# Kernel optimization log

Hardware: AMD Instinct MI355X
Metric: run time of the kernel (lower is better)

The kernel has to match this reference:

```python
import jax, jax.numpy as jnp
import numpy as np

N_NODES = 50000
N_EDGES = 800000
F_IN = 128
HID = 64
HEADS = 4
CLASSES = 40
NEG_SLOPE = 0.2
EPS = 1e-16


def glorot(key, shape):
    fan_in, fan_out = shape[0], shape[-1]
    lim = jnp.sqrt(6.0 / (fan_in + fan_out))
    return jax.random.uniform(key, shape, jnp.float32, -lim, lim)


def setup_inputs() -> dict:
    key = jax.random.key(0)
    ks = jax.random.split(key, 10)
    x = jax.random.normal(ks[0], (N_NODES, F_IN), jnp.float32)
    edge_index = jax.random.randint(ks[1], (2, N_EDGES), 0, N_NODES, jnp.int64)
    # layer 1: F_IN -> HID per head, HEADS heads, concat
    W1 = glorot(ks[2], (F_IN, HEADS * HID))
    a_src1 = glorot(ks[3], (1, HEADS, HID))
    a_dst1 = glorot(ks[4], (1, HEADS, HID))
    b1 = jnp.zeros((HEADS * HID,), jnp.float32)
    # layer 2: HEADS*HID -> CLASSES, 1 head
    W2 = glorot(ks[5], (HEADS * HID, CLASSES))
    a_src2 = glorot(ks[6], (1, 1, CLASSES))
    a_dst2 = glorot(ks[7], (1, 1, CLASSES))
    b2 = jnp.zeros((CLASSES,), jnp.float32)
    return {"x": x, "edge_index": edge_index, "W1": W1, "a_src1": a_src1,
            "a_dst1": a_dst1, "b1": b1, "W2": W2, "a_src2": a_src2,
            "a_dst2": a_dst2, "b2": b2}


def gat_conv(x, src, dst, W, a_src, a_dst, bias, heads, out_dim):
    n = x.shape[0]
    h = (x @ W).reshape(n, heads, out_dim)           # [N,H,D]
    alpha_s = jnp.sum(h * a_src, axis=-1)            # [N,H]
    alpha_d = jnp.sum(h * a_dst, axis=-1)            # [N,H]
    e = alpha_s[src] + alpha_d[dst]                  # [E,H]
    e = jax.nn.leaky_relu(e, NEG_SLOPE)
    # segment softmax over edges grouped by destination node
    m = jax.ops.segment_max(e, dst, num_segments=n)  # [N,H]
    ex = jnp.exp(e - m[dst])
    denom = jax.ops.segment_sum(ex, dst, num_segments=n)
    alpha = ex / (denom[dst] + EPS)                  # [E,H]
    msg = h[src] * alpha[:, :, None]                 # [E,H,D]
    out = jax.ops.segment_sum(msg, dst, num_segments=n)
    return out.reshape(n, heads * out_dim) + bias


def reference(x, edge_index, W1, a_src1, a_dst1, b1, W2, a_src2, a_dst2, b2):
    src, dst = edge_index[0], edge_index[1]
    h = gat_conv(x, src, dst, W1, a_src1, a_dst1, b1, HEADS, HID)
    h = jax.nn.relu(h)
    h = gat_conv(h, src, dst, W2, a_src2, a_dst2, b2, 1, CLASSES)
    return jax.nn.log_softmax(h, axis=1)
```

## Files before the change

### kernel.cpp

```cpp
#include <hip/hip_runtime.h>
#include <math.h>

#define NN 50000
#define NE 800000
#define FIN 128
#define HID 64
#define HEADS 4
#define C1 256
#define CLS 40
#define EPSF 1e-16f

#define NB 98
#define BSH 9
#define BSTRIDE 9216
#define NBLK_B 625
#define CHUNK 1280

typedef __attribute__((ext_vector_type(8))) short bf16x8;
typedef __attribute__((ext_vector_type(4))) float f32x4;
typedef __attribute__((ext_vector_type(2))) float f32x2;

__device__ __forceinline__ unsigned short f2bf(float f) {
    unsigned int u = __float_as_uint(f);
    unsigned int r = (u + 0x7fffu + ((u >> 16) & 1u)) >> 16;
    return (unsigned short)r;
}
__device__ __forceinline__ float bflo(unsigned int u) { return __uint_as_float(u << 16); }
__device__ __forceinline__ float bfhi(unsigned int u) { return __uint_as_float(u & 0xffff0000u); }
__device__ __forceinline__ unsigned char f2fp8(float v) {
    int pk = __builtin_amdgcn_cvt_pk_fp8_f32(v, v, 0, false);
    return (unsigned char)(pk & 0xff);
}
__device__ __forceinline__ float lrelu(float e) { return e > 0.f ? e : 0.2f * e; }

__global__ __launch_bounds__(512) void k_bucket(const int* __restrict__ ei,
                                                int* __restrict__ gcur,
                                                unsigned int* __restrict__ stage,
                                                const float* __restrict__ W1,
                                                const float* __restrict__ W2,
                                                unsigned short* __restrict__ wB1,
                                                unsigned short* __restrict__ wB2) {
    __shared__ unsigned int lchunk[CHUNK];
    __shared__ unsigned int lsort[CHUNK];
    __shared__ int lhist[128];
    __shared__ int sbuf[128];
    __shared__ int lstart[128];
    __shared__ int lbase[128];
    __shared__ int lcur[128];
    int t = threadIdx.x;

    if (blockIdx.x < 11) {
        int tw = blockIdx.x * 512 + t;
        if (tw < 4096) {
            int tn = tw >> 8;
            int kc = (tw >> 6) & 3;
            int lw = tw & 63;
            int n = tn * 16 + (lw & 15);
            int k0 = kc * 32 + (lw >> 4) * 8;
            unsigned short* o = wB1 + (size_t)tw * 8;
#pragma unroll
            for (int j = 0; j < 8; j++) o[j] = f2bf(W1[(size_t)(k0 + j) * C1 + n]);
        } else if (tw < 4096 + 1536) {
            int u = tw - 4096;
            int tn = u >> 9;
            int kc = (u >> 6) & 7;
            int lw = u & 63;
            int n = tn * 16 + (lw & 15);
            int k0 = kc * 32 + (lw >> 4) * 8;
            unsigned short* o = wB2 + (size_t)u * 8;
#pragma unroll
            for (int j = 0; j < 8; j++)
                o[j] = (n < CLS) ? f2bf(W2[(size_t)(k0 + j) * CLS + n]) : (unsigned short)0;
        }
    }

    int e0 = blockIdx.x * CHUNK;
    if (t < 128) lhist[t] = 0;
    __syncthreads();
    for (int j = t; j < CHUNK; j += 512) {
        int s = ei[e0 + j];
        int d = ei[NE + e0 + j];
        int b = d >> BSH;
        atomicAdd(&lhist[b], 1);
        lchunk[j] = (unsigned int)s | ((unsigned int)(d & 511) << 16) |
                    ((unsigned int)b << 25);
    }
    __syncthreads();
    if (t < 128) sbuf[t] = lhist[t];
    __syncthreads();
    for (int d = 1; d < 128; d <<= 1) {
        int x = (t < 128 && t >= d) ? sbuf[t - d] : 0;
        __syncthreads();
        if (t < 128) sbuf[t] += x;
        __syncthreads();
    }
    if (t < 128) {
        int excl = sbuf[t] - lhist[t];
        lstart[t] = excl;
        lcur[t] = excl;
        if (t < NB) lbase[t] = atomicAdd(&gcur[t], lhist[t]);
    }
    __syncthreads();
    for (int j = t; j < CHUNK; j += 512) {
        unsigned int pk = lchunk[j];
        int b = pk >> 25;
        int pos = atomicAdd(&lcur[b], 1);
        lsort[pos] = pk;
    }
    __syncthreads();
    for (int j = t; j < CHUNK; j += 512) {
        unsigned int pk = lsort[j];
        int b = pk >> 25;
        int dest = lbase[b] + (j - lstart[b]);
        stage[(size_t)b * BSTRIDE + dest] = pk & 0x01FFFFFFu;
    }
}

__global__ __launch_bounds__(512) void k_bsort(const unsigned int* __restrict__ stage,
                                               const int* __restrict__ gcur,
                                               int* __restrict__ offs,
                                               int* __restrict__ ssrc) {
    __shared__ int lhist[512];
    __shared__ int cur[512];
    __shared__ int sbuf[128];
    int t = threadIdx.x;
    int b = blockIdx.x;
    int cnt = gcur[b];
    const unsigned int* sp = stage + (size_t)b * BSTRIDE;
    if (t < 128) sbuf[t] = (t < NB) ? gcur[t] : 0;
    lhist[t] = 0;
    __syncthreads();
    for (int d = 1; d < 128; d <<= 1) {
        int x = (t < 128 && t >= d) ? sbuf[t - d] : 0;
        __syncthreads();
        if (t < 128) sbuf[t] += x;
        __syncthreads();
    }
    int gbase = sbuf[b] - cnt;
    for (int j = t; j < cnt; j += 512) atomicAdd(&lhist[(sp[j] >> 16) & 511], 1);
    __syncthreads();
    if (t < 64) {
        int base = t * 8;
        int vals[8];
        int run = 0;
#pragma unroll
        for (int j = 0; j < 8; j++) { int v = lhist[base + j]; vals[j] = run; run += v; }
        int sc = run;
#pragma unroll
        for (int d = 1; d < 64; d <<= 1) { int u = __shfl_up(sc, d); if (t >= d) sc += u; }
        int excl = sc - run;
#pragma unroll
        for (int j = 0; j < 8; j++) cur[base + j] = excl + vals[j];
    }
    __syncthreads();
    offs[(b << BSH) + t] = gbase + cur[t];
    __syncthreads();
    for (int j = t; j < cnt; j += 512) {
        unsigned int v = sp[j];
        int dl = (v >> 16) & 511;
        int pos = atomicAdd(&cur[dl], 1);
        ssrc[gbase + pos] = (int)(v & 0xFFFFu);
    }
}

__global__ __launch_bounds__(256) void k_gemm1(const float* __restrict__ x,
                                               const unsigned short* __restrict__ wB,
                                               const float* __restrict__ aws,
                                               const float* __restrict__ awd,
                                               unsigned char* __restrict__ h1f8,
                                               float* __restrict__ as1,
                                               float* __restrict__ ad1) {
    __shared__ uint4 Af[4][4][64];
    int t = threadIdx.x;
    int m0 = blockIdx.x * 64;
    int l = t & 63;
    int wv = t >> 6;

    bf16x8 bf[4][4];
    const bf16x8* wb = (const bf16x8*)wB + l;
#pragma unroll
    for (int tn = 0; tn < 4; tn++)
#pragma unroll
        for (int kc = 0; kc < 4; kc++)
            bf[tn][kc] = wb[(((wv * 4 + tn) * 4 + kc)) * 64];

#pragma unroll
    for (int i = 0; i < 8; i++) {
        int g = i * 256 + t;
        int row = g >> 5;
        int c4 = g & 31;
        int grow = m0 + row;
        if (grow >= NN) grow = NN - 1;
        float4 v = *(const float4*)(x + (size_t)grow * FIN + c4 * 4);
        uint2 pk;
        pk.x = (unsigned int)f2bf(v.x) | ((unsigned int)f2bf(v.y) << 16);
        pk.y = (unsigned int)f2bf(v.z) | ((unsigned int)f2bf(v.w) << 16);
        int kc = c4 >> 3;
        int rem = (c4 & 7) * 4;
        int q = rem >> 3;
        int hh = (rem >> 2) & 1;
        int ll = q * 16 + (row & 15);
        int mt = row >> 4;
        ((uint2*)&Af[mt][kc][ll])[hh] = pk;
    }
    __syncthreads();

    int q = l >> 4;
    int c = l & 15;

#pragma unroll
    for (int mt = 0; mt < 4; mt++) {
        bf16x8 a[4];
#pragma unroll
        for (int kc = 0; kc < 4; kc++) a[kc] = *(const bf16x8*)&Af[mt][kc][l];

        f32x4 acc[4];
#pragma unroll
        for (int tn = 0; tn < 4; tn++) acc[tn] = (f32x4){0.f, 0.f, 0.f, 0.f};
#pragma unroll
        for (int tn = 0; tn < 4; tn++) {
            acc[tn] = __builtin_amdgcn_mfma_f32_16x16x32_bf16(a[0], bf[tn][0], acc[tn], 0, 0, 0);
            acc[tn] = __builtin_amdgcn_mfma_f32_16x16x32_bf16(a[1], bf[tn][1], acc[tn], 0, 0, 0);
            acc[tn] = __builtin_amdgcn_mfma_f32_16x16x32_bf16(a[2], bf[tn][2], acc[tn], 0, 0, 0);
            acc[tn] = __builtin_amdgcn_mfma_f32_16x16x32_bf16(a[3], bf[tn][3], acc[tn], 0, 0, 0);
        }

        int row0 = m0 + mt * 16 + q * 4;
        float ps[4] = {0.f, 0.f, 0.f, 0.f}, pd[4] = {0.f, 0.f, 0.f, 0.f};
#pragma unroll
        for (int tn = 0; tn < 4; tn++) {
            int col = wv * 64 + tn * 16 + c;
            float wsv = aws[col];
            float wdv = awd[col];
#pragma unroll
            for (int r = 0; r < 4; r++) {
                float v = acc[tn][r];
                int row = row0 + r;
                if (row < NN) h1f8[(size_t)row * C1 + col] = f2fp8(v);
                ps[r] = fmaf(v, wsv, ps[r]);
                pd[r] = fmaf(v, wdv, pd[r]);
            }
        }
#pragma unroll
        for (int r = 0; r < 4; r++) {
            float a_ = ps[r], d_ = pd[r];
#pragma unroll
            for (int s = 1; s < 16; s <<= 1) {
                a_ += __shfl_xor(a_, s);
                d_ += __shfl_xor(d_, s);
            }
            int row = row0 + r;
            if (c == 0 && row < NN) {
                as1[row * 4 + wv] = a_;
                ad1[row * 4 + wv] = d_;
            }
        }
    }
}

__global__ __launch_bounds__(256) void k_agg1(const unsigned char* __restrict__ h1f8,
                                              const float* __restrict__ as1,
                                              const float* __restrict__ ad1,
                                              const int* __restrict__ offs,
                                              const int* __restrict__ ssrc,
                                              const float* __restrict__ b1,
                                              unsigned short* __restrict__ g1b) {
    int lane = threadIdx.x & 63;
    int half = lane >> 5;
    int hl = lane & 31;
    int head = hl >> 3;
    int node = blockIdx.x * 4 + (threadIdx.x >> 6);
    int beg = offs[node];
    int end = (node + 1 < NN) ? offs[node + 1] : NE;
    float adv = ad1[node * 4 + head];
    float l = 0.f;
    float acc[8];
#pragma unroll
    for (int c = 0; c < 8; c++) acc[c] = 0.f;
    const uint2* hv = (const uint2*)h1f8;

    if (beg < end) {
        int idx[4];
#pragma unroll
        for (int i = 0; i < 4; i++) idx[i] = ssrc[beg + 2 * i + half];
        uint2 hbA[2];
        float pA[2];
#pragma unroll
        for (int i = 0; i < 2; i++) {
            hbA[i] = hv[(size_t)idx[i] * 32 + hl];
            int e = beg + 2 * i + half;
            float p = __expf(lrelu(as1[idx[i] * 4 + head] + adv));
            pA[i] = (e < end) ? p : 0.f;
        }
        for (int j = beg; j < end; j += 8) {
            int idxN[4];
#pragma unroll
            for (int i = 0; i < 4; i++) idxN[i] = ssrc[j + 8 + 2 * i + half];
            uint2 hbB[2];
            float pB[2];
#pragma unroll
            for (int i = 0; i < 2; i++) {
                hbB[i] = hv[(size_t)idx[2 + i] * 32 + hl];
                int e = j + 4 + 2 * i + half;
                float p = __expf(lrelu(as1[idx[2 + i] * 4 + head] + adv));
                pB[i] = (e < end) ? p : 0.f;
            }
#pragma unroll
            for (int i = 0; i < 2; i++) {
                float p = pA[i];
                f32x2 v0 = __builtin_amdgcn_cvt_pk_f32_fp8(hbA[i].x, false);
                f32x2 v1 = __builtin_amdgcn_cvt_pk_f32_fp8(hbA[i].x, true);
                f32x2 v2 = __builtin_amdgcn_cvt_pk_f32_fp8(hbA[i].y, false);
                f32x2 v3 = __builtin_amdgcn_cvt_pk_f32_fp8(hbA[i].y, true);
                l += p;
                acc[0] = fmaf(p, v0.x, acc[0]);
                acc[1] = fmaf(p, v0.y, acc[1]);
                acc[2] = fmaf(p, v1.x, acc[2]);
                acc[3] = fmaf(p, v1.y, acc[3]);
                acc[4] = fmaf(p, v2.x, acc[4]);
                acc[5] = fmaf(p, v2.y, acc[5]);
                acc[6] = fmaf(p, v3.x, acc[6]);
                acc[7] = fmaf(p, v3.y, acc[7]);
            }
#pragma unroll
            for (int i = 0; i < 2; i++) {
                hbA[i] = hv[(size_t)idxN[i] * 32 + hl];
                int e = j + 8 + 2 * i + half;
                float p = __expf(lrelu(as1[idxN[i] * 4 + head] + adv));
                pA[i] = (e < end) ? p : 0.f;
            }
#pragma unroll
            for (int i = 0; i < 2; i++) {
                float p = pB[i];
                f32x2 v0 = __builtin_amdgcn_cvt_pk_f32_fp8(hbB[i].x, false);
                f32x2 v1 = __builtin_amdgcn_cvt_pk_f32_fp8(hbB[i].x, true);
                f32x2 v2 = __builtin_amdgcn_cvt_pk_f32_fp8(hbB[i].y, false);
                f32x2 v3 = __builtin_amdgcn_cvt_pk_f32_fp8(hbB[i].y, true);
                l += p;
                acc[0] = fmaf(p, v0.x, acc[0]);
                acc[1] = fmaf(p, v0.y, acc[1]);
                acc[2] = fmaf(p, v1.x, acc[2]);
                acc[3] = fmaf(p, v1.y, acc[3]);
                acc[4] = fmaf(p, v2.x, acc[4]);
                acc[5] = fmaf(p, v2.y, acc[5]);
                acc[6] = fmaf(p, v3.x, acc[6]);
                acc[7] = fmaf(p, v3.y, acc[7]);
            }
#pragma unroll
            for (int i = 0; i < 4; i++) idx[i] = idxN[i];
        }
    }
    l += __shfl_xor(l, 32);
#pragma unroll
    for (int c = 0; c < 8; c++) acc[c] += __shfl_xor(acc[c], 32);

    if (half == 0) {
        float inv = 1.f / (l + EPSF);
        const float4* b1v = (const float4*)b1;
        float4 b0 = b1v[hl * 2];
        float4 b1_ = b1v[hl * 2 + 1];
        float o[8];
        o[0] = fmaxf(fmaf(acc[0], inv, b0.x), 0.f);
        o[1] = fmaxf(fmaf(acc[1], inv, b0.y), 0.f);
        o[2] = fmaxf(fmaf(acc[2], inv, b0.z), 0.f);
        o[3] = fmaxf(fmaf(acc[3], inv, b0.w), 0.f);
        o[4] = fmaxf(fmaf(acc[4], inv, b1_.x), 0.f);
        o[5] = fmaxf(fmaf(acc[5], inv, b1_.y), 0.f);
        o[6] = fmaxf(fmaf(acc[6], inv, b1_.z), 0.f);
        o[7] = fmaxf(fmaf(acc[7], inv, b1_.w), 0.f);
        uint4 ob;
        ob.x = (unsigned int)f2bf(o[0]) | ((unsigned int)f2bf(o[1]) << 16);
        ob.y = (unsigned int)f2bf(o[2]) | ((unsigned int)f2bf(o[3]) << 16);
        ob.z = (unsigned int)f2bf(o[4]) | ((unsigned int)f2bf(o[5]) << 16);
        ob.w = (unsigned int)f2bf(o[6]) | ((unsigned int)f2bf(o[7]) << 16);
        ((uint4*)g1b)[(size_t)node * 32 + hl] = ob;
    }
}

__global__ __launch_bounds__(256) void k_gemm2(const unsigned short* __restrict__ g1b,
                                               const unsigned short* __restrict__ wB2,
                                               const float* __restrict__ aws,
                                               const float* __restrict__ awd,
                                               unsigned short* __restrict__ h2b,
                                               float* __restrict__ as2,
                                               float* __restrict__ ad2) {
    __shared__ uint4 Af[4][8][64];
    int t = threadIdx.x;
    int m0 = blockIdx.x * 64;

#pragma unroll
    for (int i = 0; i < 8; i++) {
        int g = i * 256 + t;
        int row = g >> 5;
        int c8 = g & 31;
        int grow = m0 + row;
        if (grow >= NN) grow = NN - 1;
        uint4 v = *(const uint4*)(g1b + (size_t)grow * C1 + c8 * 8);
        int kc = c8 >> 2;
        int q = c8 & 3;
        Af[row >> 4][kc][q * 16 + (row & 15)] = v;
    }
    __syncthreads();

    int l = t & 63;
    int wv = t >> 6;

    bf16x8 a[8];
#pragma unroll
    for (int kc = 0; kc < 8; kc++) a[kc] = *(const bf16x8*)&Af[wv][kc][l];

    f32x4 acc[3];
#pragma unroll
    for (int tn = 0; tn < 3; tn++) acc[tn] = (f32x4){0.f, 0.f, 0.f, 0.f};

    const bf16x8* wb = (const bf16x8*)wB2 + l;
#pragma unroll
    for (int tn = 0; tn < 3; tn++) {
#pragma unroll
        for (int kc = 0; kc < 8; kc++) {
            bf16x8 b = wb[(tn * 8 + kc) * 64];
            acc[tn] = __builtin_amdgcn_mfma_f32_16x16x32_bf16(a[kc], b, acc[tn], 0, 0, 0);
        }
    }

    int q = l >> 4;
    int c = l & 15;
    int row0 = m0 + wv * 16 + q * 4;
    float ps[4] = {0.f, 0.f, 0.f, 0.f}, pd[4] = {0.f, 0.f, 0.f, 0.f};
#pragma unroll
    for (int tn = 0; tn < 3; tn++) {
        int col = tn * 16 + c;
        bool cok = col < CLS;
        float wsv = cok ? aws[col] : 0.f;
        float wdv = cok ? awd[col] : 0.f;
#pragma unroll
        for (int r = 0; r < 4; r++) {
            float v = acc[tn][r];
            int row = row0 + r;
            if (cok && row < NN) h2b[(size_t)row * CLS + col] = f2bf(v);
            ps[r] = fmaf(v, wsv, ps[r]);
            pd[r] = fmaf(v, wdv, pd[r]);
        }
    }
#pragma unroll
    for (int r = 0; r < 4; r++) {
        float a_ = ps[r], d_ = pd[r];
#pragma unroll
        for (int s = 1; s < 16; s <<= 1) {
            a_ += __shfl_xor(a_, s);
            d_ += __shfl_xor(d_, s);
        }
        int row = row0 + r;
        if (c == 0 && row < NN) {
            as2[row] = a_;
            ad2[row] = d_;
        }
    }
}

__global__ __launch_bounds__(256) void k_agg2(const unsigned short* __restrict__ h2b,
                                              const float* __restrict__ as2,
                                              const float* __restrict__ ad2,
                                              const int* __restrict__ offs,
                                              const int* __restrict__ ssrc,
                                              const float* __restrict__ b2,
                                              float* __restrict__ out) {
    int lane = threadIdx.x & 63;
    int half = lane >> 5;
    int hl = lane & 31;
    int cl = hl < 20 ? hl : 19;
    int node = blockIdx.x * 4 + (threadIdx.x >> 6);
    int beg = offs[node];
    int end = (node + 1 < NN) ? offs[node + 1] : NE;
    float adv = ad2[node];
    float l = 0.f, aL = 0.f, aH = 0.f;
    const unsigned int* hv = (const unsigned int*)h2b;

    if (beg < end) {
        int idx[4];
#pragma unroll
        for (int i = 0; i < 4; i++) idx[i] = ssrc[beg + 2 * i + half];
        unsigned int hbA[2];
        float pA[2];
#pragma unroll
        for (int i = 0; i < 2; i++) {
            hbA[i] = hv[(size_t)idx[i] * 20 + cl];
            int e = beg + 2 * i + half;
            float p = __expf(lrelu(as2[idx[i]] + adv));
            pA[i] = (e < end) ? p : 0.f;
        }
        for (int j = beg; j < end; j += 8) {
            int idxN[4];
#pragma unroll
            for (int i = 0; i < 4; i++) idxN[i] = ssrc[j + 8 + 2 * i + half];
            unsigned int hbB[2];
            float pB[2];
#pragma unroll
            for (int i = 0; i < 2; i++) {
                hbB[i] = hv[(size_t)idx[2 + i] * 20 + cl];
                int e = j + 4 + 2 * i + half;
                float p = __expf(lrelu(as2[idx[2 + i]] + adv));
                pB[i] = (e < end) ? p : 0.f;
            }
#pragma unroll
            for (int i = 0; i < 2; i++) {
                float p = pA[i];
                l += p;
                aL = fmaf(p, bflo(hbA[i]), aL);
                aH = fmaf(p, bfhi(hbA[i]), aH);
            }
#pragma unroll
            for (int i = 0; i < 2; i++) {
                hbA[i] = hv[(size_t)idxN[i] * 20 + cl];
                int e = j + 8 + 2 * i + half;
                float p = __expf(lrelu(as2[idxN[i]] + adv));
                pA[i] = (e < end) ? p : 0.f;
            }
#pragma unroll
            for (int i = 0; i < 2; i++) {
                float p = pB[i];
                l += p;
                aL = fmaf(p, bflo(hbB[i]), aL);
                aH = fmaf(p, bfhi(hbB[i]), aH);
            }
#pragma unroll
            for (int i = 0; i < 4; i++) idx[i] = idxN[i];
        }
    }
    l += __shfl_xor(l, 32);
    aL += __shfl_xor(aL, 32);
    aH += __shfl_xor(aH, 32);

    if (half == 0) {
        bool act = hl < 20;
        float inv = 1.f / (l + EPSF);
        float vL = -INFINITY, vH = -INFINITY;
        if (act) {
            float2 b = ((const float2*)b2)[cl];
            vL = aL * inv + b.x;
            vH = aH * inv + b.y;
        }
        float mx = fmaxf(vL, vH);
#pragma unroll
        for (int s = 16; s >= 1; s >>= 1) mx = fmaxf(mx, __shfl_xor(mx, s));
        float ex = act ? (__expf(vL - mx) + __expf(vH - mx)) : 0.f;
#pragma unroll
        for (int s = 16; s >= 1; s >>= 1) ex += __shfl_xor(ex, s);
        if (act) {
            float ls = __logf(ex);
            float2 o = {vL - mx - ls, vH - mx - ls};
            *(float2*)(out + (size_t)node * CLS + cl * 2) = o;
        }
    }
}


extern "C" void kernel_launch(void* const* d_in, const int* in_sizes, int n_in,
                              void* d_out, int out_size, void* d_ws, size_t ws_size,
                              hipStream_t stream) {
    const float* x    = (const float*)d_in[0];
    const int*   ei   = (const int*)d_in[1];
    const float* W1   = (const float*)d_in[2];
    const float* as1w = (const float*)d_in[3];
    const float* ad1w = (const float*)d_in[4];
    const float* b1   = (const float*)d_in[5];
    const float* W2   = (const float*)d_in[6];
    const float* as2w = (const float*)d_in[7];
    const float* ad2w = (const float*)d_in[8];
    const float* b2   = (const float*)d_in[9];
    float* out = (float*)d_out;

    char* p = (char*)d_ws;
    auto alloc = [&](size_t bytes) {
        char* r = p;
        p += (bytes + 255) & ~(size_t)255;
        return r;
    };
    unsigned char* h1f8 = (unsigned char*)alloc((size_t)NN * C1);
    unsigned short* g1b = (unsigned short*)alloc((size_t)NN * C1 * 2);
    unsigned short* h2b = (unsigned short*)alloc((size_t)NN * CLS * 2);
    float* as1  = (float*)alloc((size_t)NN * 4 * 4);
    float* ad1  = (float*)alloc((size_t)NN * 4 * 4);
    float* as2  = (float*)alloc((size_t)NN * 4);
    float* ad2  = (float*)alloc((size_t)NN * 4);
    int* offs   = (int*)alloc((size_t)(NN + 1024) * 4);
    int* gcur   = (int*)alloc(128 * 4);
    unsigned int* stage = (unsigned int*)alloc((size_t)NB * BSTRIDE * 4);
    int* ssrc   = (int*)alloc((size_t)(NE + 64) * 4);
    unsigned short* wB1 = (unsigned short*)alloc((size_t)4096 * 8 * 2);
    unsigned short* wB2 = (unsigned short*)alloc((size_t)1536 * 8 * 2);

    hipMemsetAsync(gcur, 0, 128 * 4, stream);
    hipMemsetAsync(ssrc + NE, 0, 64 * 4, stream);

    k_bucket<<<NBLK_B, 512, 0, stream>>>(ei, gcur, stage, W1, W2, wB1, wB2);
    k_bsort<<<NB, 512, 0, stream>>>(stage, gcur, offs, ssrc);

    k_gemm1<<<(NN + 63) / 64, 256, 0, stream>>>(x, wB1, as1w, ad1w, h1f8, as1, ad1);
    k_agg1<<<NN / 4, 256, 0, stream>>>(h1f8, as1, ad1, offs, ssrc, b1, g1b);

    k_gemm2<<<(NN + 63) / 64, 256, 0, stream>>>(g1b, wB2, as2w, ad2w, h2b, as2, ad2);
    k_agg2<<<NN / 4, 256, 0, stream>>>(h2b, as2, ad2, offs, ssrc, b2, out);
}
```

Before: 213.9 us.

## Split layer-1 aggregation per head and pin each head to an XCD pair

The layer-1 aggregation now launches one wave per (node, head) instead of one wave per node covering all heads. The block index is decoded so that all blocks for a given head land on the same pair of XCDs, which keeps each head's 64-byte slice of the fp8 feature table resident in those XCDs' L2. Each wave processes 8 edges per iteration with 8 lanes per edge, then reduces across lane groups with shuffles. The cost is four times as many blocks, repeated loads of offsets, edge indices and attention scores for every head, and extra shuffle reductions.

```diff
diff --git a/kernel.cpp b/kernel.cpp
--- a/kernel.cpp
+++ b/kernel.cpp
@@ -266,99 +266,67 @@
                                               const float* __restrict__ b1,
                                               unsigned short* __restrict__ g1b) {
     int lane = threadIdx.x & 63;
-    int half = lane >> 5;
-    int hl = lane & 31;
-    int head = hl >> 3;
-    int node = blockIdx.x * 4 + (threadIdx.x >> 6);
+    int g = lane >> 3;
+    int c = lane & 7;
+    int bid = blockIdx.x;
+    int xcd = bid & 7;
+    int head = xcd >> 1;
+    int quad = (bid >> 3) * 2 + (bid & 1);
+    int node = quad * 4 + (threadIdx.x >> 6);
     int beg = offs[node];
     int end = (node + 1 < NN) ? offs[node + 1] : NE;
     float adv = ad1[node * 4 + head];
     float l = 0.f;
     float acc[8];
 #pragma unroll
-    for (int c = 0; c < 8; c++) acc[c] = 0.f;
-    const uint2* hv = (const uint2*)h1f8;
+    for (int k = 0; k < 8; k++) acc[k] = 0.f;
+    const uint2* hv = (const uint2*)(h1f8 + head * 64);
+
+#define ACC1(hb, p)                                                       \
+    {                                                                     \
+        f32x2 v;                                                          \
+        v = __builtin_amdgcn_cvt_pk_f32_fp8((hb).x, false);               \
+        acc[0] = fmaf(p, v.x, acc[0]); acc[1] = fmaf(p, v.y, acc[1]);     \
+        v = __builtin_amdgcn_cvt_pk_f32_fp8((hb).x, true);                \
+        acc[2] = fmaf(p, v.x, acc[2]); acc[3] = fmaf(p, v.y, acc[3]);     \
+        v = __builtin_amdgcn_cvt_pk_f32_fp8((hb).y, false);               \
+        acc[4] = fmaf(p, v.x, acc[4]); acc[5] = fmaf(p, v.y, acc[5]);     \
+        v = __builtin_amdgcn_cvt_pk_f32_fp8((hb).y, true);                \
+        acc[6] = fmaf(p, v.x, acc[6]); acc[7] = fmaf(p, v.y, acc[7]);     \
+        l += p;                                                           \
+    }
 
     if (beg < end) {
-        int idx[4];
-#pragma unroll
-        for (int i = 0; i < 4; i++) idx[i] = ssrc[beg + 2 * i + half];
-        uint2 hbA[2];
-        float pA[2];
-#pragma unroll
-        for (int i = 0; i < 2; i++) {
-            hbA[i] = hv[(size_t)idx[i] * 32 + hl];
-            int e = beg + 2 * i + half;
-            float p = __expf(lrelu(as1[idx[i] * 4 + head] + adv));
-            pA[i] = (e < end) ? p : 0.f;
-        }
+        int eA = beg + g;
+        int iA = ssrc[eA];
+        uint2 hA = hv[(size_t)iA * 32 + c];
+        float pA = (eA < end) ? __expf(lrelu(as1[iA * 4 + head] + adv)) : 0.f;
         for (int j = beg; j < end; j += 8) {
-            int idxN[4];
-#pragma unroll
-            for (int i = 0; i < 4; i++) idxN[i] = ssrc[j + 8 + 2 * i + half];
-            uint2 hbB[2];
-            float pB[2];
-#pragma unroll
-            for (int i = 0; i < 2; i++) {
-                hbB[i] = hv[(size_t)idx[2 + i] * 32 + hl];
-                int e = j + 4 + 2 * i + half;
-                float p = __expf(lrelu(as1[idx[2 + i] * 4 + head] + adv));
-                pB[i] = (e < end) ? p : 0.f;
-            }
-#pragma unroll
-            for (int i = 0; i < 2; i++) {
-                float p = pA[i];
-                f32x2 v0 = __builtin_amdgcn_cvt_pk_f32_fp8(hbA[i].x, false);
-                f32x2 v1 = __builtin_amdgcn_cvt_pk_f32_fp8(hbA[i].x, true);
-                f32x2 v2 = __builtin_amdgcn_cvt_pk_f32_fp8(hbA[i].y, false);
-                f32x2 v3 = __builtin_amdgcn_cvt_pk_f32_fp8(hbA[i].y, true);
-                l += p;
-                acc[0] = fmaf(p, v0.x, acc[0]);
-                acc[1] = fmaf(p, v0.y, acc[1]);
-                acc[2] = fmaf(p, v1.x, acc[2]);
-                acc[3] = fmaf(p, v1.y, acc[3]);
-                acc[4] = fmaf(p, v2.x, acc[4]);
-                acc[5] = fmaf(p, v2.y, acc[5]);
-                acc[6] = fmaf(p, v3.x, acc[6]);
-                acc[7] = fmaf(p, v3.y, acc[7]);
-            }
-#pragma unroll
-            for (int i = 0; i < 2; i++) {
-                hbA[i] = hv[(size_t)idxN[i] * 32 + hl];
-                int e = j + 8 + 2 * i + half;
-                float p = __expf(lrelu(as1[idxN[i] * 4 + head] + adv));
-                pA[i] = (e < end) ? p : 0.f;
-            }
-#pragma unroll
-            for (int i = 0; i < 2; i++) {
-                float p = pB[i];
-                f32x2 v0 = __builtin_amdgcn_cvt_pk_f32_fp8(hbB[i].x, false);
-                f32x2 v1 = __builtin_amdgcn_cvt_pk_f32_fp8(hbB[i].x, true);
-                f32x2 v2 = __builtin_amdgcn_cvt_pk_f32_fp8(hbB[i].y, false);
-                f32x2 v3 = __builtin_amdgcn_cvt_pk_f32_fp8(hbB[i].y, true);
-                l += p;
-                acc[0] = fmaf(p, v0.x, acc[0]);
-                acc[1] = fmaf(p, v0.y, acc[1]);
-                acc[2] = fmaf(p, v1.x, acc[2]);
-                acc[3] = fmaf(p, v1.y, acc[3]);
-                acc[4] = fmaf(p, v2.x, acc[4]);
-                acc[5] = fmaf(p, v2.y, acc[5]);
-                acc[6] = fmaf(p, v3.x, acc[6]);
-                acc[7] = fmaf(p, v3.y, acc[7]);
-            }
-#pragma unroll
-            for (int i = 0; i < 4; i++) idx[i] = idxN[i];
-        }
-    }
+            int eB = j + 8 + g;
+            int iB = ssrc[eB];
+            uint2 hB = hv[(size_t)iB * 32 + c];
+            float pB = (eB < end) ? __expf(lrelu(as1[iB * 4 + head] + adv)) : 0.f;
+            ACC1(hA, pA);
+            hA = hB;
+            pA = pB;
+        }
+    }
+#undef ACC1
+#pragma unroll
+    for (int k = 0; k < 8; k++) acc[k] += __shfl_xor(acc[k], 8);
+    l += __shfl_xor(l, 8);
+#pragma unroll
+    for (int k = 0; k < 8; k++) acc[k] += __shfl_xor(acc[k], 16);
+    l += __shfl_xor(l, 16);
+#pragma unroll
+    for (int k = 0; k < 8; k++) acc[k] += __shfl_xor(acc[k], 32);
     l += __shfl_xor(l, 32);
-#pragma unroll
-    for (int c = 0; c < 8; c++) acc[c] += __shfl_xor(acc[c], 32);
-
-    if (half == 0) {
+
+    if (g == 0) {
         float inv = 1.f / (l + EPSF);
         const float4* b1v = (const float4*)b1;
-        float4 b0 = b1v[hl * 2];
-        float4 b1_ = b1v[hl * 2 + 1];
+        float4 b0 = b1v[head * 16 + c * 2];
+        float4 b1_ = b1v[head * 16 + c * 2 + 1];
         float o[8];
         o[0] = fmaxf(fmaf(acc[0], inv, b0.x), 0.f);
         o[1] = fmaxf(fmaf(acc[1], inv, b0.y), 0.f);
@@ -373,7 +341,7 @@
         ob.y = (unsigned int)f2bf(o[2]) | ((unsigned int)f2bf(o[3]) << 16);
         ob.z = (unsigned int)f2bf(o[4]) | ((unsigned int)f2bf(o[5]) << 16);
         ob.w = (unsigned int)f2bf(o[6]) | ((unsigned int)f2bf(o[7]) << 16);
-        ((uint4*)g1b)[(size_t)node * 32 + hl] = ob;
+        ((uint4*)g1b)[(size_t)node * 32 + head * 8 + c] = ob;
     }
 }
 
@@ -597,7 +565,7 @@
     k_bsort<<<NB, 512, 0, stream>>>(stage, gcur, offs, ssrc);
 
     k_gemm1<<<(NN + 63) / 64, 256, 0, stream>>>(x, wB1, as1w, ad1w, h1f8, as1, ad1);
-    k_agg1<<<NN / 4, 256, 0, stream>>>(h1f8, as1, ad1, offs, ssrc, b1, g1b);
+    k_agg1<<<(NN / 4) * HEADS, 256, 0, stream>>>(h1f8, as1, ad1, offs, ssrc, b1, g1b);
 
     k_gemm2<<<(NN + 63) / 64, 256, 0, stream>>>(g1b, wB2, as2w, ad2w, h2b, as2, ad2);
     k_agg2<<<NN / 4, 256, 0, stream>>>(h2b, as2, ad2, offs, ssrc, b2, out);
```

Result: slower. 282.3 us (+31.9%).

## Merge bucket sort and first GEMM into one heterogeneous launch

Applied to the files above, without the earlier changes.

Fuses the per-bucket CSR sort kernel and the layer-1 GEMM into a single launch. The first NB blocks do the sort and the rest do GEMM tiles, two 64-row tiles per 512-thread block, with a shared-memory union covering both roles. The aim is to run the small 98-block sort alongside the independent GEMM and save one launch gap. The GEMM path now uses 512-thread blocks, which may change occupancy, and its trailing block reads clamped rows past NN.

```diff
diff --git a/kernel.cpp b/kernel.cpp
--- a/kernel.cpp
+++ b/kernel.cpp
@@ -15,6 +15,7 @@
 #define BSTRIDE 9216
 #define NBLK_B 625
 #define CHUNK 1280
+#define NBLK_G 391
 
 typedef __attribute__((ext_vector_type(8))) short bf16x8;
 typedef __attribute__((ext_vector_type(4))) float f32x4;
@@ -116,63 +117,67 @@
     }
 }
 
-__global__ __launch_bounds__(512) void k_bsort(const unsigned int* __restrict__ stage,
-                                               const int* __restrict__ gcur,
-                                               int* __restrict__ offs,
-                                               int* __restrict__ ssrc) {
-    __shared__ int lhist[512];
-    __shared__ int cur[512];
-    __shared__ int sbuf[128];
-    int t = threadIdx.x;
-    int b = blockIdx.x;
-    int cnt = gcur[b];
-    const unsigned int* sp = stage + (size_t)b * BSTRIDE;
-    if (t < 128) sbuf[t] = (t < NB) ? gcur[t] : 0;
-    lhist[t] = 0;
-    __syncthreads();
-    for (int d = 1; d < 128; d <<= 1) {
-        int x = (t < 128 && t >= d) ? sbuf[t - d] : 0;
+__global__ __launch_bounds__(512) void k_bsg(const unsigned int* __restrict__ stage,
+                                             const int* __restrict__ gcur,
+                                             int* __restrict__ offs,
+                                             int* __restrict__ ssrc,
+                                             const float* __restrict__ x,
+                                             const unsigned short* __restrict__ wB,
+                                             const float* __restrict__ aws,
+                                             const float* __restrict__ awd,
+                                             unsigned char* __restrict__ h1f8,
+                                             float* __restrict__ as1,
+                                             float* __restrict__ ad1) {
+    __shared__ union SM {
+        struct { int lhist[512]; int cur[512]; int sbuf[128]; } b;
+        struct { uint4 Af[2][4][4][64]; } g;
+    } sm;
+
+    if (blockIdx.x < NB) {
+        int t = threadIdx.x;
+        int b = blockIdx.x;
+        int cnt = gcur[b];
+        const unsigned int* sp = stage + (size_t)b * BSTRIDE;
+        if (t < 128) sm.b.sbuf[t] = (t < NB) ? gcur[t] : 0;
+        sm.b.lhist[t] = 0;
         __syncthreads();
-        if (t < 128) sbuf[t] += x;
+        for (int d = 1; d < 128; d <<= 1) {
+            int xv = (t < 128 && t >= d) ? sm.b.sbuf[t - d] : 0;
+            __syncthreads();
+            if (t < 128) sm.b.sbuf[t] += xv;
+            __syncthreads();
+        }
+        int gbase = sm.b.sbuf[b] - cnt;
+        for (int j = t; j < cnt; j += 512) atomicAdd(&sm.b.lhist[(sp[j] >> 16) & 511], 1);
         __syncthreads();
-    }
-    int gbase = sbuf[b] - cnt;
-    for (int j = t; j < cnt; j += 512) atomicAdd(&lhist[(sp[j] >> 16) & 511], 1);
-    __syncthreads();
-    if (t < 64) {
-        int base = t * 8;
-        int vals[8];
-        int run = 0;
-#pragma unroll
-        for (int j = 0; j < 8; j++) { int v = lhist[base + j]; vals[j] = run; run += v; }
-        int sc = run;
-#pragma unroll
-        for (int d = 1; d < 64; d <<= 1) { int u = __shfl_up(sc, d); if (t >= d) sc += u; }
-        int excl = sc - run;
-#pragma unroll
-        for (int j = 0; j < 8; j++) cur[base + j] = excl + vals[j];
-    }
-    __syncthreads();
-    offs[(b << BSH) + t] = gbase + cur[t];
-    __syncthreads();
-    for (int j = t; j < cnt; j += 512) {
-        unsigned int v = sp[j];
-        int dl = (v >> 16) & 511;
-        int pos = atomicAdd(&cur[dl], 1);
-        ssrc[gbase + pos] = (int)(v & 0xFFFFu);
-    }
-}
-
-__global__ __launch_bounds__(256) void k_gemm1(const float* __restrict__ x,
-                                               const unsigned short* __restrict__ wB,
-                                               const float* __restrict__ aws,
-                                               const float* __restrict__ awd,
-                                               unsigned char* __restrict__ h1f8,
-                                               float* __restrict__ as1,
-                                               float* __restrict__ ad1) {
-    __shared__ uint4 Af[4][4][64];
-    int t = threadIdx.x;
-    int m0 = blockIdx.x * 64;
+        if (t < 64) {
+            int base = t * 8;
+            int vals[8];
+            int run = 0;
+#pragma unroll
+            for (int j = 0; j < 8; j++) { int v = sm.b.lhist[base + j]; vals[j] = run; run += v; }
+            int sc = run;
+#pragma unroll
+            for (int d = 1; d < 64; d <<= 1) { int u = __shfl_up(sc, d); if (t >= d) sc += u; }
+            int excl = sc - run;
+#pragma unroll
+            for (int j = 0; j < 8; j++) sm.b.cur[base + j] = excl + vals[j];
+        }
+        __syncthreads();
+        offs[(b << BSH) + t] = gbase + sm.b.cur[t];
+        __syncthreads();
+        for (int j = t; j < cnt; j += 512) {
+            unsigned int v = sp[j];
+            int dl = (v >> 16) & 511;
+            int pos = atomicAdd(&sm.b.cur[dl], 1);
+            ssrc[gbase + pos] = (int)(v & 0xFFFFu);
+        }
+        return;
+    }
+
+    int half = threadIdx.x >> 8;
+    int t = threadIdx.x & 255;
+    int m0 = ((blockIdx.x - NB) * 2 + half) * 64;
     int l = t & 63;
     int wv = t >> 6;
 
@@ -201,7 +206,7 @@
         int hh = (rem >> 2) & 1;
         int ll = q * 16 + (row & 15);
         int mt = row >> 4;
-        ((uint2*)&Af[mt][kc][ll])[hh] = pk;
+        ((uint2*)&sm.g.Af[half][mt][kc][ll])[hh] = pk;
     }
     __syncthreads();
 
@@ -212,7 +217,7 @@
     for (int mt = 0; mt < 4; mt++) {
         bf16x8 a[4];
 #pragma unroll
-        for (int kc = 0; kc < 4; kc++) a[kc] = *(const bf16x8*)&Af[mt][kc][l];
+        for (int kc = 0; kc < 4; kc++) a[kc] = *(const bf16x8*)&sm.g.Af[half][mt][kc][l];
 
         f32x4 acc[4];
 #pragma unroll
@@ -594,9 +599,8 @@
     hipMemsetAsync(ssrc + NE, 0, 64 * 4, stream);
 
     k_bucket<<<NBLK_B, 512, 0, stream>>>(ei, gcur, stage, W1, W2, wB1, wB2);
-    k_bsort<<<NB, 512, 0, stream>>>(stage, gcur, offs, ssrc);
-
-    k_gemm1<<<(NN + 63) / 64, 256, 0, stream>>>(x, wB1, as1w, ad1w, h1f8, as1, ad1);
+    k_bsg<<<NB + NBLK_G, 512, 0, stream>>>(stage, gcur, offs, ssrc,
+                                           x, wB1, as1w, ad1w, h1f8, as1, ad1);
     k_agg1<<<NN / 4, 256, 0, stream>>>(h1f8, as1, ad1, offs, ssrc, b1, g1b);
 
     k_gemm2<<<(NN + 63) / 64, 256, 0, stream>>>(g1b, wB2, as2w, ad2w, h2b, as2, ad2);
```

After: 198.6 us. 1.08x faster.
